# Performance work log

Hardware: AMD Instinct MI355X
Metric: run time of the kernel (lower is better)

The kernel has to match this reference:

```python
import jax, jax.numpy as jnp
import numpy as np

N_GRAPHS, GRAPH_SIZE = 64, 1024
N = N_GRAPHS * GRAPH_SIZE
IN_DIM, WIDTH, EMB, PROP, SPACE, K, NCONV = 34, 126, 128, 32, 4, 8, 5
NUM_CLASSES = 8


def _mlp4(x, W1, b1, W23, b23, W4, b4):
    h = jax.nn.elu(x @ W1 + b1)
    h = jax.nn.elu(h @ W23[0] + b23[0])
    h = jax.nn.elu(h @ W23[1] + b23[1])
    return h @ W4 + b4


def _gravnet(x, Wh, bh, Ws, bs, Wo, bo):
    # x: (N, EMB). GravNetConv: project to learned space, kNN within each graph,
    # messages h_j * exp(-10*d^2), aggregate [mean, max], concat with x, linear.
    h = x @ Wh + bh                                   # (N, PROP)
    s = x @ Ws + bs                                   # (N, SPACE)
    sg = s.reshape(N_GRAPHS, GRAPH_SIZE, SPACE)
    hg = h.reshape(N_GRAPHS, GRAPH_SIZE, PROP)
    sn2 = jnp.sum(sg * sg, -1)                        # (G,S)
    d2 = sn2[:, :, None] + sn2[:, None, :] - 2.0 * jnp.einsum('gid,gjd->gij', sg, sg)
    _, idx = jax.lax.top_k(-jax.lax.stop_gradient(d2), K)   # (G,S,K) incl. self
    s_nb = jax.vmap(lambda a, i: a[i])(sg, idx)       # (G,S,K,SPACE)
    h_nb = jax.vmap(lambda a, i: a[i])(hg, idx)       # (G,S,K,PROP)
    d2k = jnp.sum((sg[:, :, None, :] - s_nb) ** 2, -1)
    w = jnp.exp(-10.0 * d2k)                          # (G,S,K)
    msg = h_nb * w[..., None]
    agg = jnp.concatenate([msg.mean(2), msg.max(2)], -1).reshape(N, 2 * PROP)
    return jnp.concatenate([x, agg], -1) @ Wo + bo    # (N, EMB)


def _run_convs(emb, Wh, bh, Ws, bs, Wo, bo):
    # params have leading dim NCONV; convs are chained (layer i feeds layer i+1)
    def step(carry, p):
        out = _gravnet(carry, *p)
        return out, out
    _, outs = jax.lax.scan(step, emb, (Wh, bh, Ws, bs, Wo, bo))
    return outs  # (NCONV, N, EMB)


def _forward(x, n0W1, n0b1, n0W23, n0b23, n0W4, n0b4,
             cWh, cbh, cWs, cbs, cWo, cbo,
             HW1, Hb1, HW23, Hb23, Wid, bid, Wreg, breg, Wch, bch):
    emb = _mlp4(x, n0W1, n0b1, n0W23, n0b23, n0W4, n0b4)   # (N, EMB)
    # two independent conv stacks (id, reg) share the embedding input
    outs = jax.vmap(_run_convs, in_axes=(None, 0, 0, 0, 0, 0, 0))(
        emb, cWh, cbh, cWs, cbs, cWo, cbo)                  # (2, NCONV, N, EMB)
    f_id = jnp.concatenate([x, outs[0].transpose(1, 0, 2).reshape(N, NCONV * EMB)], -1)
    f_rg = jnp.concatenate([x, outs[1].transpose(1, 0, 2).reshape(N, NCONV * EMB)], -1)
    preds_id = _mlp4(f_id, HW1[0], Hb1[0], HW23[0], Hb23[0], Wid, bid)
    preds_mom = _mlp4(f_rg, HW1[1], Hb1[1], HW23[1], Hb23[1], Wreg, breg) + x[:, 1:5]
    pred_charge = _mlp4(f_rg, HW1[2], Hb1[2], HW23[2], Hb23[2], Wch, bch)
    return preds_id, preds_mom, pred_charge


def setup_inputs() -> dict:
    key = jax.random.key(0)
    ks = jax.random.split(key, 16)
    def W(i, shape):
        return jax.random.normal(ks[i], shape, jnp.float32) / np.float32(np.sqrt(shape[-2]))
    def b(shape):
        return jnp.zeros(shape, jnp.float32)
    FEAT = IN_DIM + NCONV * EMB
    return dict(
        x=jax.random.normal(ks[0], (N, IN_DIM), jnp.float32),
        batch=(jnp.arange(N) // GRAPH_SIZE).astype(jnp.int32),
        n0W1=W(1, (IN_DIM, WIDTH)), n0b1=b((WIDTH,)),
        n0W23=W(2, (2, WIDTH, WIDTH)), n0b23=b((2, WIDTH)),
        n0W4=W(3, (WIDTH, EMB)), n0b4=b((EMB,)),
        cWh=W(4, (2, NCONV, EMB, PROP)), cbh=b((2, NCONV, PROP)),
        cWs=W(5, (2, NCONV, EMB, SPACE)), cbs=b((2, NCONV, SPACE)),
        cWo=W(6, (2, NCONV, EMB + 2 * PROP, EMB)), cbo=b((2, NCONV, EMB)),
        HW1=W(7, (3, FEAT, WIDTH)), Hb1=b((3, WIDTH)),
        HW23=W(8, (3, 2, WIDTH, WIDTH)), Hb23=b((3, 2, WIDTH)),
        Wid=W(9, (WIDTH, NUM_CLASSES)), bid=b((NUM_CLASSES,)),
        Wreg=W(10, (WIDTH, 4)), breg=b((4,)),
        Wch=W(11, (WIDTH, 1)), bch=b((1,)),
    )


def reference(x, batch, n0W1, n0b1, n0W23, n0b23, n0W4, n0b4,
              cWh, cbh, cWs, cbs, cWo, cbo,
              HW1, Hb1, HW23, Hb23, Wid, bid, Wreg, breg, Wch, bch):
    # `batch` is implied by the fixed (N_GRAPHS, GRAPH_SIZE) layout used in _gravnet
    return _forward(x, n0W1, n0b1, n0W23, n0b23, n0W4, n0b4,
                    cWh, cbh, cWs, cbs, cWo, cbo,
                    HW1, Hb1, HW23, Hb23, Wid, bid, Wreg, breg, Wch, bch)
```

## Files before the change

kernel.cpp:

```cpp
#include <hip/hip_runtime.h>
#include <hip/hip_bf16.h>
#include <cstdint>

#define N_TOT 65536
#define NG 64
#define GS 1024
#define IN_DIM 34
#define WIDTH 126
#define EMB 128
#define PROP 32
#define SPACE 4
#define KNN 8
#define NCONV 5
#define FEAT (IN_DIM + NCONV*EMB)
#define FLDB 680
#define CATW (EMB + 2*PROP)
#define AGGW (2*PROP)
#define PRJW 36

typedef __attribute__((ext_vector_type(8))) short short8v;
typedef __attribute__((ext_vector_type(4))) float f32x4;

__device__ __forceinline__ unsigned short f2bf(float f){
  unsigned int u = __float_as_uint(f);
  unsigned int r = (u + 0x7FFFu + ((u >> 16) & 1u)) >> 16;
  return (unsigned short)r;
}
__device__ __forceinline__ float bf2f(unsigned short b){
  return __uint_as_float(((unsigned int)b) << 16);
}

struct WDesc {
  const float* s1; const float* s2;
  int ld1, ld2, nc1, K, Nn, limbs, ncp;
  long long dstoff;
};
#define NMAT 32
struct WDescs { WDesc d[NMAT]; };

__global__ __launch_bounds__(256)
void conv_weights_kernel(WDescs DS, unsigned short* __restrict__ pool)
{
  int m = blockIdx.y;
  WDesc d = DS.d[m];
  if (d.K == 0) return;
  int ntiles = (d.K + 31) >> 5;
  int ncp = d.ncp;
  int nchunk = ncp >> 5;
  int kt = blockIdx.x / nchunk;
  int cc = blockIdx.x % nchunk;
  if (kt >= ntiles) return;
  int t = threadIdx.x;
  int kk = t & 31;
  int k = kt*32 + kk;
  for (int c = (t >> 5); c < 32; c += 8){
    int col = cc*32 + c;
    float v = 0.f;
    if (k < d.K && col < d.Nn)
      v = (col < d.nc1) ? d.s1[(size_t)k*d.ld1 + col]
                        : d.s2[(size_t)k*d.ld2 + (col - d.nc1)];
    for (int l = 0; l < d.limbs; ++l){
      unsigned short b = f2bf(v); v -= bf2f(b);
      pool[d.dstoff + ((long long)(l*ntiles + kt)*ncp + col)*32 + kk] = b;
    }
  }
}

__global__ __launch_bounds__(256)
void xconv_kernel(const float* __restrict__ x, unsigned short* __restrict__ featb)
{
  int idx = blockIdx.x*256 + threadIdx.x;
  if (idx < N_TOT*IN_DIM){
    int r = idx / IN_DIM, c = idx - r*IN_DIM;
    featb[(size_t)r*FLDB + c] = f2bf(x[idx]);
  }
}

template<int LIMBS, int ABF, int NT>
__global__ __launch_bounds__(256)
void mfma_gemm(const void* __restrict__ A1v, int lda1, int K1,
               const float* __restrict__ A2, int lda2, int K2,
               const unsigned short* __restrict__ BL, int ncp,
               const float* __restrict__ bias1, const float* __restrict__ bias2,
               int bsplit,
               float* __restrict__ C, int ldc, int Nn, int mode, int act,
               unsigned short* __restrict__ Cb, int ldcb)
{
  constexpr int ASTR = LIMBS*32 + 8;
  constexpr int RB = (NT == 128) ? 4 : 2;
  __shared__ __align__(16) unsigned short Alds[128*ASTR];
  const float* A1 = (const float*)A1v;
  const unsigned short* Ab = (const unsigned short*)A1v;

  const int K = K1 + K2;
  const int ntiles = (K + 31) >> 5;
  const int t = threadIdx.x;
  const int bm0 = blockIdx.x * 128;
  const int col0 = blockIdx.y * NT;
  const int lane = t & 63;
  const int wid  = t >> 6;
  const int wr = (NT == 128) ? (wid >> 1) * 64 : wid * 32;
  const int wc = (NT == 128) ? (wid & 1) * 64 : 0;
  const int frow = lane & 15;
  const int fk   = (lane >> 4) * 8;
  const int a_row = t >> 1;
  const int a_kh  = (t & 1) * 16;
  const size_t rr = (size_t)(bm0 + a_row);

  float v[16];
  short8v pb0, pb1;

  auto loadreg = [&](int kt){
    const int k0 = kt * 32;
    if (ABF){
      if (k0 + 31 < K){
        pb0 = *(const short8v*)&Ab[rr*lda1 + k0 + a_kh];
        pb1 = *(const short8v*)&Ab[rr*lda1 + k0 + a_kh + 8];
      } else {
        #pragma unroll
        for (int j = 0; j < 8; ++j){
          int ka = k0 + a_kh + j;
          pb0[j] = (ka < K) ? (short)Ab[rr*lda1 + ka] : (short)0;
        }
        #pragma unroll
        for (int j = 0; j < 8; ++j){
          int ka = k0 + a_kh + 8 + j;
          pb1[j] = (ka < K) ? (short)Ab[rr*lda1 + ka] : (short)0;
        }
      }
    } else {
      #pragma unroll
      for (int j = 0; j < 16; ++j){
        int ka = k0 + a_kh + j;
        float xv = 0.f;
        if (ka < K)
          xv = (ka < K1) ? A1[rr*lda1 + ka] : A2[rr*lda2 + (ka - K1)];
        v[j] = xv;
      }
    }
  };

  auto storelds = [&](){
    if (ABF){
      *(short8v*)&Alds[a_row*ASTR + a_kh]     = pb0;
      *(short8v*)&Alds[a_row*ASTR + a_kh + 8] = pb1;
    } else {
      #pragma unroll
      for (int l = 0; l < LIMBS; ++l){
        short8v q0, q1;
        #pragma unroll
        for (int j = 0; j < 8; ++j){
          unsigned short b = f2bf(v[j]); v[j] -= bf2f(b); q0[j] = (short)b;
        }
        #pragma unroll
        for (int j = 0; j < 8; ++j){
          unsigned short b = f2bf(v[8+j]); v[8+j] -= bf2f(b); q1[j] = (short)b;
        }
        *(short8v*)&Alds[a_row*ASTR + l*32 + a_kh]     = q0;
        *(short8v*)&Alds[a_row*ASTR + l*32 + a_kh + 8] = q1;
      }
    }
  };

  f32x4 acc[RB][4];
  #pragma unroll
  for (int i = 0; i < RB; ++i)
    #pragma unroll
    for (int j = 0; j < 4; ++j)
      acc[i][j] = (f32x4){0.f, 0.f, 0.f, 0.f};

  loadreg(0);
  for (int kt = 0; kt < ntiles; ++kt){
    __syncthreads();
    storelds();
    if (kt + 1 < ntiles) loadreg(kt + 1);
    __syncthreads();
    #pragma unroll
    for (int lA = 0; lA < LIMBS; ++lA){
      short8v af[RB];
      #pragma unroll
      for (int rb = 0; rb < RB; ++rb)
        af[rb] = *(const short8v*)&Alds[(wr + rb*16 + frow)*ASTR + lA*32 + fk];
      #pragma unroll
      for (int lB = 0; lB < LIMBS - lA; ++lB){
        const unsigned short* bbase =
            BL + ((long long)(lB*ntiles + kt)*ncp)*32;
        short8v bfr[4];
        #pragma unroll
        for (int cb = 0; cb < 4; ++cb){
          int col = col0 + wc + cb*16 + frow;
          bfr[cb] = *(const short8v*)&bbase[(long long)col*32 + fk];
        }
        #pragma unroll
        for (int rb = 0; rb < RB; ++rb)
          #pragma unroll
          for (int cb = 0; cb < 4; ++cb)
            acc[rb][cb] = __builtin_amdgcn_mfma_f32_16x16x32_bf16(
                af[rb], bfr[cb], acc[rb][cb], 0, 0, 0);
      }
    }
  }

  const int lr4 = (lane >> 4) * 4;
  #pragma unroll
  for (int rb = 0; rb < RB; ++rb){
    #pragma unroll
    for (int cb = 0; cb < 4; ++cb){
      const int col = col0 + wc + cb*16 + frow;
      if (col < Nn){
        float bv = 0.f;
        if (bias1) bv = (col < bsplit) ? bias1[col] : bias2[col - bsplit];
        #pragma unroll
        for (int ri = 0; ri < 4; ++ri){
          const size_t row = (size_t)(bm0 + wr + rb*16 + lr4 + ri);
          float vv = acc[rb][cb][ri];
          if (mode == 1){
            C[row*ldc + col] += vv;
          } else if (mode == 2){
            float a2 = vv + C[row*ldc + col] + bv;
            C[row*ldc + col] = (a2 > 0.f) ? a2 : expm1f(a2);
          } else {
            if (bias1) vv += bv;
            if (act == 1) vv = (vv > 0.f) ? vv : expm1f(vv);
            C[row*ldc + col] = vv;
            if (Cb) Cb[row*(size_t)ldcb + col] = f2bf(vv);
          }
        }
      }
    }
  }
}

template<int BM, int BN, int BK, int TM, int TN>
__global__ __launch_bounds__(256)
void gemm_tile_kernel(const float* __restrict__ A1, int lda1, int K1,
                      const float* __restrict__ W, const float* __restrict__ bias,
                      float* __restrict__ C, int ldc, int Nn, int act,
                      const float* __restrict__ addx, int addx_ld, int addx_off)
{
  constexpr int LDA = BM + 4;
  constexpr int LDB = BN + 4;
  constexpr int APASS = (BM*BK)/1024;
  constexpr int BPASS = (BN*BK)/1024;
  constexpr int AROWS = 256/(BK/4);
  constexpr int BROWS = 256/(BN/4);
  __shared__ float As[BK*LDA];
  __shared__ float Bs[BK*LDB];
  const int K = K1;
  const int t = threadIdx.x;
  const int bm0 = blockIdx.x * BM;
  const int bn0 = blockIdx.y * BN;
  const int tx = t % 16;
  const int ty = t / 16;
  const int a_r = t / (BK/4);
  const int a_k = 4 * (t % (BK/4));
  const int b_c = t % (BN/4);
  const int b_k = t / (BN/4);

  float ar[APASS][4], br[BPASS][4];
  auto load_tile = [&](int k0){
    #pragma unroll
    for (int p = 0; p < APASS; ++p){
      size_t rr = (size_t)(bm0 + a_r + p*AROWS);
      #pragma unroll
      for (int j = 0; j < 4; ++j){
        int ka = k0 + a_k + j;
        ar[p][j] = (ka < K) ? A1[rr*lda1 + ka] : 0.f;
      }
    }
    #pragma unroll
    for (int p = 0; p < BPASS; ++p){
      int kb = k0 + b_k + p*BROWS;
      #pragma unroll
      for (int j = 0; j < 4; ++j){
        int col = bn0 + 4*b_c + j;
        br[p][j] = (kb < K && col < Nn) ? W[(size_t)kb*Nn + col] : 0.f;
      }
    }
  };
  auto store_tile = [&](){
    #pragma unroll
    for (int p = 0; p < APASS; ++p)
      #pragma unroll
      for (int j = 0; j < 4; ++j)
        As[(a_k + j)*LDA + a_r + p*AROWS] = ar[p][j];
    #pragma unroll
    for (int p = 0; p < BPASS; ++p)
      *(float4*)&Bs[(b_k + p*BROWS)*LDB + 4*b_c] =
          make_float4(br[p][0], br[p][1], br[p][2], br[p][3]);
  };

  float acc[TM][TN];
  #pragma unroll
  for (int i = 0; i < TM; ++i)
    #pragma unroll
    for (int j = 0; j < TN; ++j) acc[i][j] = 0.f;

  auto compute_tile = [&](){
    #pragma unroll
    for (int kk = 0; kk < BK; ++kk){
      float a[TM], b[TN];
      #pragma unroll
      for (int iq = 0; iq < TM/4; ++iq){
        float4 v = *(const float4*)&As[kk*LDA + iq*(BM/2) + 4*ty];
        a[iq*4+0] = v.x; a[iq*4+1] = v.y; a[iq*4+2] = v.z; a[iq*4+3] = v.w;
      }
      #pragma unroll
      for (int jq = 0; jq < TN/4; ++jq){
        float4 v = *(const float4*)&Bs[kk*LDB + jq*(BN/2) + 4*tx];
        b[jq*4+0] = v.x; b[jq*4+1] = v.y; b[jq*4+2] = v.z; b[jq*4+3] = v.w;
      }
      #pragma unroll
      for (int i = 0; i < TM; ++i)
        #pragma unroll
        for (int j = 0; j < TN; ++j)
          acc[i][j] += a[i]*b[j];
    }
  };

  const int ntiles = (K + BK - 1)/BK;
  load_tile(0); store_tile(); __syncthreads();
  for (int tt = 1; tt < ntiles; ++tt){
    load_tile(tt*BK);
    compute_tile();
    __syncthreads();
    store_tile();
    __syncthreads();
  }
  compute_tile();

  #pragma unroll
  for (int i = 0; i < TM; ++i){
    size_t row = (size_t)(bm0 + (i/4)*(BM/2) + 4*ty + (i%4));
    #pragma unroll
    for (int j = 0; j < TN; ++j){
      int col = bn0 + (j/4)*(BN/2) + 4*tx + (j%4);
      if (col < Nn){
        float v = acc[i][j];
        if (bias) v += bias[col];
        if (act == 1) v = (v > 0.f) ? v : expm1f(v);
        if (addx) v += addx[row*addx_ld + addx_off + col];
        C[row*ldc + col] = v;
      }
    }
  }
}

__global__ __launch_bounds__(256)
void knn_agg_kernel(const float* __restrict__ proj, float* __restrict__ agg)
{
  __shared__ float4 ssv[GS];
  __shared__ float  sn2[GS];
  __shared__ float  cd[4][64][KNN];
  __shared__ int    ci[4][64][KNN];
  __shared__ float  wl[64][KNN];

  const int g   = blockIdx.x >> 4;
  const int seg = blockIdx.x & 15;
  const int t = threadIdx.x;
  const int wave = t >> 6;
  const int lane = t & 63;

  const float* pg = proj + (size_t)g*GS*PRJW;
  for (int i = t; i < GS; i += 256){
    float4 v = *(const float4*)(pg + (size_t)i*PRJW + PROP);
    ssv[i] = v;
    sn2[i] = v.x*v.x + v.y*v.y + v.z*v.z + v.w*v.w;
  }
  __syncthreads();

  const int i = seg*64 + lane;
  float4 sv = ssv[i];
  float myn2 = sn2[i];
  float si0 = sv.x, si1 = sv.y, si2 = sv.z, si3 = sv.w;

  float bd[KNN]; int bi[KNN];
  #pragma unroll
  for (int k = 0; k < KNN; ++k){ bd[k] = 1e30f; bi[k] = 0; }

  const int jbeg = wave * 256;
  for (int j0 = jbeg; j0 < jbeg + 256; j0 += 8){
    float dv[8];
    #pragma unroll
    for (int u = 0; u < 8; ++u){
      float4 sj = ssv[j0+u];
      float dot = si0*sj.x + si1*sj.y + si2*sj.z + si3*sj.w;
      dv[u] = myn2 + sn2[j0+u] - 2.f*dot;
    }
    float mn = fminf(fminf(fminf(dv[0],dv[1]), fminf(dv[2],dv[3])),
                     fminf(fminf(dv[4],dv[5]), fminf(dv[6],dv[7])));
    if (mn < bd[KNN-1]){
      #pragma unroll
      for (int u = 0; u < 8; ++u){
        float d2 = dv[u];
        if (d2 < bd[KNN-1]){
          int j = j0 + u;
          #pragma unroll
          for (int q = KNN-1; q >= 1; --q){
            bool cq = d2 < bd[q];
            bool cp = d2 < bd[q-1];
            float nv = cp ? bd[q-1] : d2;
            int   ni = cp ? bi[q-1] : j;
            if (cq){ bd[q] = nv; bi[q] = ni; }
          }
          if (d2 < bd[0]){ bd[0] = d2; bi[0] = j; }
        }
      }
    }
  }
  #pragma unroll
  for (int k = 0; k < KNN; ++k){ cd[wave][lane][k] = bd[k]; ci[wave][lane][k] = bi[k]; }
  __syncthreads();

  if (wave == 0){
    #pragma unroll
    for (int c = 1; c < 4; ++c){
      #pragma unroll
      for (int k = 0; k < KNN; ++k){
        float d2 = cd[c][lane][k];
        if (d2 < bd[KNN-1]){
          int j = ci[c][lane][k];
          #pragma unroll
          for (int q = KNN-1; q >= 1; --q){
            bool cq = d2 < bd[q];
            bool cp = d2 < bd[q-1];
            float nv = cp ? bd[q-1] : d2;
            int   ni = cp ? bi[q-1] : j;
            if (cq){ bd[q] = nv; bi[q] = ni; }
          }
          if (d2 < bd[0]){ bd[0] = d2; bi[0] = j; }
        }
      }
    }
    #pragma unroll
    for (int k = 0; k < KNN; ++k){ cd[0][lane][k] = bd[k]; ci[0][lane][k] = bi[k]; }
  }
  __syncthreads();

  {
    const int r = t & 63;
    float4 si_ = ssv[seg*64 + r];
    #pragma unroll
    for (int kx = (t >> 6); kx < KNN; kx += 4){
      int j = ci[0][r][kx];
      float4 sj = ssv[j];
      float d0 = si_.x - sj.x, d1 = si_.y - sj.y;
      float d2_ = si_.z - sj.z, d3 = si_.w - sj.w;
      float dd = d0*d0 + d1*d1 + d2_*d2_ + d3*d3;
      wl[r][kx] = expf(-10.f*dd);
    }
  }
  __syncthreads();

  {
    const int r = t & 63;
    const int q = t >> 6;
    float msum[8], mmax[8];
    #pragma unroll
    for (int u = 0; u < 8; ++u){ msum[u] = 0.f; mmax[u] = -1e30f; }
    #pragma unroll
    for (int k = 0; k < KNN; ++k){
      int j = ci[0][r][k];
      float wk = wl[r][k];
      const float* hr = pg + (size_t)j*PRJW + q*8;
      float4 h0 = *(const float4*)(hr);
      float4 h1 = *(const float4*)(hr + 4);
      float v0 = h0.x*wk, v1 = h0.y*wk, v2 = h0.z*wk, v3 = h0.w*wk;
      float v4 = h1.x*wk, v5 = h1.y*wk, v6 = h1.z*wk, v7 = h1.w*wk;
      msum[0]+=v0; mmax[0]=fmaxf(mmax[0],v0);
      msum[1]+=v1; mmax[1]=fmaxf(mmax[1],v1);
      msum[2]+=v2; mmax[2]=fmaxf(mmax[2],v2);
      msum[3]+=v3; mmax[3]=fmaxf(mmax[3],v3);
      msum[4]+=v4; mmax[4]=fmaxf(mmax[4],v4);
      msum[5]+=v5; mmax[5]=fmaxf(mmax[5],v5);
      msum[6]+=v6; mmax[6]=fmaxf(mmax[6],v6);
      msum[7]+=v7; mmax[7]=fmaxf(mmax[7],v7);
    }
    float* arow = agg + ((size_t)g*GS + seg*64 + r)*AGGW;
    #pragma unroll
    for (int u = 0; u < 8; ++u){
      arow[q*8 + u]        = msum[u]*(1.f/KNN);
      arow[PROP + q*8 + u] = mmax[u];
    }
  }
}

extern "C" void kernel_launch(void* const* d_in, const int* in_sizes, int n_in,
                              void* d_out, int out_size, void* d_ws, size_t ws_size,
                              hipStream_t stream)
{
  const float* x     = (const float*)d_in[0];
  const float* n0W1  = (const float*)d_in[2];
  const float* n0b1  = (const float*)d_in[3];
  const float* n0W23 = (const float*)d_in[4];
  const float* n0b23 = (const float*)d_in[5];
  const float* n0W4  = (const float*)d_in[6];
  const float* n0b4  = (const float*)d_in[7];
  const float* cWh   = (const float*)d_in[8];
  const float* cbh   = (const float*)d_in[9];
  const float* cWs   = (const float*)d_in[10];
  const float* cbs   = (const float*)d_in[11];
  const float* cWo   = (const float*)d_in[12];
  const float* cbo   = (const float*)d_in[13];
  const float* HW1   = (const float*)d_in[14];
  const float* Hb1   = (const float*)d_in[15];
  const float* HW23  = (const float*)d_in[16];
  const float* Hb23  = (const float*)d_in[17];
  const float* Wid   = (const float*)d_in[18];
  const float* bid   = (const float*)d_in[19];
  const float* Wreg  = (const float*)d_in[20];
  const float* breg  = (const float*)d_in[21];
  const float* Wch   = (const float*)d_in[22];
  const float* bch   = (const float*)d_in[23];
  float* out = (float*)d_out;
  (void)in_sizes; (void)n_in; (void)out_size;

  char* wsp = (char*)d_ws;
  unsigned short* featb = (unsigned short*)(wsp);
  float* P     = (float*)(wsp + 89128960);
  float* Q     = (float*)(wsp + 122683392);
  float* projb = (float*)(wsp + 156237824);
  float* aggb  = (float*)(wsp + 165675008);
  unsigned short* pool = (unsigned short*)(wsp + 182452224);
  float* hacc  = P;
  float* t1    = (float*)wsp;

  WDescs DS{};
  long long woff = 0; int nd = 0;
  auto addm = [&](const float* s1, const float* s2, int ld1, int ld2,
                  int nc1, int K, int Nn, int limbs, int nalign)->long long {
    int ntiles = (K + 31) >> 5;
    int ncp = (Nn + nalign - 1) & ~(nalign - 1);
    long long o = woff;
    DS.d[nd].s1 = s1; DS.d[nd].s2 = s2; DS.d[nd].ld1 = ld1; DS.d[nd].ld2 = ld2;
    DS.d[nd].nc1 = nc1; DS.d[nd].K = K; DS.d[nd].Nn = Nn; DS.d[nd].limbs = limbs;
    DS.d[nd].ncp = ncp; DS.d[nd].dstoff = o; nd++;
    woff += (long long)limbs * ntiles * ncp * 32;
    return o;
  };
  long long o_e1 = addm(n0W1, nullptr, WIDTH, 0, WIDTH, IN_DIM, WIDTH, 3, 128);
  long long o_e2 = addm(n0W23, nullptr, WIDTH, 0, WIDTH, WIDTH, WIDTH, 3, 128);
  long long o_e3 = addm(n0W23 + WIDTH*WIDTH, nullptr, WIDTH, 0, WIDTH, WIDTH, WIDTH, 3, 128);
  long long o_e4 = addm(n0W4, nullptr, EMB, 0, EMB, WIDTH, EMB, 3, 128);
  long long o_pj[10], o_wo[10];
  for (int p = 0; p < 10; ++p){
    o_pj[p] = addm(cWh + (size_t)p*EMB*PROP, cWs + (size_t)p*EMB*SPACE,
                   PROP, SPACE, PROP, EMB, PRJW, 3, 64);
    o_wo[p] = addm(cWo + (size_t)p*CATW*EMB, nullptr, EMB, 0, EMB, CATW, EMB, 3, 128);
  }
  long long o_L1s0  = addm(HW1, nullptr, WIDTH, 0, WIDTH, FEAT, WIDTH, 1, 128);
  long long o_L1s12 = addm(HW1 + (size_t)1*FEAT*WIDTH, HW1 + (size_t)2*FEAT*WIDTH,
                           WIDTH, WIDTH, WIDTH, FEAT, 2*WIDTH, 1, 128);
  long long o_hh[6];
  for (int q = 0; q < 6; ++q)
    o_hh[q] = addm(HW23 + (size_t)q*WIDTH*WIDTH, nullptr, WIDTH, 0, WIDTH, WIDTH, WIDTH, 1, 128);

  long long E_off = ((182452224LL + woff*2) + 255) & ~255LL;
  bool haveE = (E_off + (long long)N_TOT*EMB*4 <= (long long)ws_size);
  float* E = (float*)(wsp + E_off);

  hipLaunchKernelGGL(conv_weights_kernel, dim3(176, NMAT), dim3(256), 0, stream, DS, pool);

  auto gemmM = [&](int limbs, int abf, int nt, const void* A1, int lda1, int K1,
                   const float* A2, int lda2, int K2,
                   long long boff, int ncp,
                   const float* b1, const float* b2, int bsplit,
                   float* C, int ldc, int Nn, int mode, int act,
                   unsigned short* Cb, int ldcb){
    dim3 grid(N_TOT/128, ncp/nt);
    if (limbs == 3 && nt == 64)
      hipLaunchKernelGGL((mfma_gemm<3,0,64>), grid, dim3(256), 0, stream,
          A1, lda1, K1, A2, lda2, K2, pool + boff, ncp, b1, b2, bsplit,
          C, ldc, Nn, mode, act, Cb, ldcb);
    else if (limbs == 3)
      hipLaunchKernelGGL((mfma_gemm<3,0,128>), grid, dim3(256), 0, stream,
          A1, lda1, K1, A2, lda2, K2, pool + boff, ncp, b1, b2, bsplit,
          C, ldc, Nn, mode, act, Cb, ldcb);
    else if (abf)
      hipLaunchKernelGGL((mfma_gemm<1,1,128>), grid, dim3(256), 0, stream,
          A1, lda1, K1, A2, lda2, K2, pool + boff, ncp, b1, b2, bsplit,
          C, ldc, Nn, mode, act, Cb, ldcb);
    else
      hipLaunchKernelGGL((mfma_gemm<1,0,128>), grid, dim3(256), 0, stream,
          A1, lda1, K1, A2, lda2, K2, pool + boff, ncp, b1, b2, bsplit,
          C, ldc, Nn, mode, act, Cb, ldcb);
  };
  auto gemmS = [&](const float* A1, int lda1, int K1,
                   const float* W, const float* b,
                   float* C, int ldc, int Nn, int act,
                   const float* addx, int addx_ld, int addx_off){
    dim3 grid(N_TOT/64, (Nn+63)/64);
    hipLaunchKernelGGL((gemm_tile_kernel<64,64,32,4,4>), grid, dim3(256), 0, stream,
        A1, lda1, K1, W, b, C, ldc, Nn, act, addx, addx_ld, addx_off);
  };
  const int BIG = 1 << 30;

  auto run_embedding = [&](float* dst){
    gemmM(3,0,128, x, IN_DIM, IN_DIM, nullptr,0,0, o_e1, 128, n0b1, nullptr, BIG,
          Q, EMB, WIDTH, 0, 1, nullptr, 0);
    gemmM(3,0,128, Q, EMB, WIDTH, nullptr,0,0, o_e2, 128, n0b23, nullptr, BIG,
          P, EMB, WIDTH, 0, 1, nullptr, 0);
    gemmM(3,0,128, P, EMB, WIDTH, nullptr,0,0, o_e3, 128, n0b23 + WIDTH, nullptr, BIG,
          Q, EMB, WIDTH, 0, 1, nullptr, 0);
    gemmM(3,0,128, Q, EMB, WIDTH, nullptr,0,0, o_e4, 128, n0b4, nullptr, BIG,
          dst, EMB, EMB, 0, 0, nullptr, 0);
  };

  if (haveE) run_embedding(E);

  for (int s = 0; s < 2; ++s){
    hipLaunchKernelGGL(xconv_kernel, dim3((N_TOT*IN_DIM + 255)/256), dim3(256),
                       0, stream, x, featb);
    if (!haveE) run_embedding(P);

    float* cur = haveE ? E : P;
    float* b0  = haveE ? P : Q;
    float* b1  = haveE ? Q : P;

    for (int cv = 0; cv < NCONV; ++cv){
      int pidx = s*NCONV + cv;
      float* nxt = (cv & 1) ? b1 : b0;
      gemmM(3,0,64, cur, EMB, EMB, nullptr,0,0, o_pj[pidx], 64,
            cbh + pidx*PROP, cbs + pidx*SPACE, PROP,
            projb, PRJW, PRJW, 0, 0, nullptr, 0);
      hipLaunchKernelGGL(knn_agg_kernel, dim3(NG*16), dim3(256), 0, stream,
                         projb, aggb);
      gemmM(3,0,128, cur, EMB, EMB, aggb, AGGW, AGGW, o_wo[pidx], 128,
            cbo + pidx*EMB, nullptr, BIG, nxt, EMB, EMB, 0, 0,
            featb + IN_DIM + cv*EMB, FLDB);
      cur = nxt;
    }

    if (s == 0){
      gemmM(1,1,128, featb, FLDB, FEAT, nullptr,0,0, o_L1s0, 128,
            Hb1, nullptr, BIG, hacc, WIDTH, WIDTH, 0, 1, nullptr, 0);
    } else {
      gemmM(1,1,128, featb, FLDB, FEAT, nullptr,0,0, o_L1s12, 256,
            Hb1 + WIDTH, Hb1 + 2*WIDTH, WIDTH,
            hacc, 2*WIDTH, 2*WIDTH, 0, 1, nullptr, 0);
    }

    auto finish_head = [&](int hidx, float* ha, int lda_ha,
                           float* dst, int dst_ld, int out_dim,
                           const float* Wl, const float* bl,
                           const float* addx, int addx_ld, int addx_off){
      gemmM(1,0,128, ha, lda_ha, WIDTH, nullptr,0,0, o_hh[hidx*2+0], 128,
            Hb23 + (hidx*2+0)*WIDTH, nullptr, BIG,
            t1, WIDTH, WIDTH, 0, 1, nullptr, 0);
      gemmM(1,0,128, t1, WIDTH, WIDTH, nullptr,0,0, o_hh[hidx*2+1], 128,
            Hb23 + (hidx*2+1)*WIDTH, nullptr, BIG,
            ha, lda_ha, WIDTH, 0, 1, nullptr, 0);
      gemmS(ha, lda_ha, WIDTH, Wl, bl, dst, dst_ld, out_dim, 0,
            addx, addx_ld, addx_off);
    };

    if (s == 0){
      finish_head(0, hacc, WIDTH, out, 8, 8, Wid, bid, nullptr, 0, 0);
    } else {
      finish_head(1, hacc, 2*WIDTH, out + (size_t)N_TOT*8, 4, 4,
                  Wreg, breg, x, IN_DIM, 1);
      finish_head(2, hacc + WIDTH, 2*WIDTH, out + (size_t)N_TOT*12, 1, 1,
                  Wch, bch, nullptr, 0, 0);
    }
  }
}
```

Baseline: 2.355 ms.

## Fuse Wo GEMM with next-layer projection and shrink MFMA GEMM row tile

Adds a fused kernel that computes the GravNet output linear layer and then, from the result kept in LDS as three bf16 limbs, the next conv's h/s projection. This removes one separate projection GEMM launch per conv and the re-read of the new embedding from global memory. The generic MFMA GEMM row tile drops from 128 to 64 rows per block and the unused accumulate modes are removed, giving more blocks and less LDS per block at the cost of more B-fragment reloads. The knn kernel's block-to-graph mapping is also reordered so consecutive blocks cover different graphs.

```diff
diff --git a/kernel.cpp b/kernel.cpp
--- a/kernel.cpp
+++ b/kernel.cpp
@@ -18,15 +18,16 @@
 #define AGGW (2*PROP)
 #define PRJW 36
 
+typedef unsigned short ushort;
 typedef __attribute__((ext_vector_type(8))) short short8v;
 typedef __attribute__((ext_vector_type(4))) float f32x4;
 
-__device__ __forceinline__ unsigned short f2bf(float f){
+__device__ __forceinline__ ushort f2bf(float f){
   unsigned int u = __float_as_uint(f);
   unsigned int r = (u + 0x7FFFu + ((u >> 16) & 1u)) >> 16;
-  return (unsigned short)r;
+  return (ushort)r;
 }
-__device__ __forceinline__ float bf2f(unsigned short b){
+__device__ __forceinline__ float bf2f(ushort b){
   return __uint_as_float(((unsigned int)b) << 16);
 }
 
@@ -39,7 +40,7 @@
 struct WDescs { WDesc d[NMAT]; };
 
 __global__ __launch_bounds__(256)
-void conv_weights_kernel(WDescs DS, unsigned short* __restrict__ pool)
+void conv_weights_kernel(WDescs DS, ushort* __restrict__ pool)
 {
   int m = blockIdx.y;
   WDesc d = DS.d[m];
@@ -60,14 +61,14 @@
       v = (col < d.nc1) ? d.s1[(size_t)k*d.ld1 + col]
                         : d.s2[(size_t)k*d.ld2 + (col - d.nc1)];
     for (int l = 0; l < d.limbs; ++l){
-      unsigned short b = f2bf(v); v -= bf2f(b);
+      ushort b = f2bf(v); v -= bf2f(b);
       pool[d.dstoff + ((long long)(l*ntiles + kt)*ncp + col)*32 + kk] = b;
     }
   }
 }
 
 __global__ __launch_bounds__(256)
-void xconv_kernel(const float* __restrict__ x, unsigned short* __restrict__ featb)
+void xconv_kernel(const float* __restrict__ x, ushort* __restrict__ featb)
 {
   int idx = blockIdx.x*256 + threadIdx.x;
   if (idx < N_TOT*IN_DIM){
@@ -80,57 +81,51 @@
 __global__ __launch_bounds__(256)
 void mfma_gemm(const void* __restrict__ A1v, int lda1, int K1,
                const float* __restrict__ A2, int lda2, int K2,
-               const unsigned short* __restrict__ BL, int ncp,
+               const ushort* __restrict__ BL, int ncp,
                const float* __restrict__ bias1, const float* __restrict__ bias2,
                int bsplit,
-               float* __restrict__ C, int ldc, int Nn, int mode, int act,
-               unsigned short* __restrict__ Cb, int ldcb)
+               float* __restrict__ C, int ldc, int Nn, int act,
+               ushort* __restrict__ Cb, int ldcb)
 {
   constexpr int ASTR = LIMBS*32 + 8;
-  constexpr int RB = (NT == 128) ? 4 : 2;
-  __shared__ __align__(16) unsigned short Alds[128*ASTR];
+  constexpr int CB = (NT == 128) ? 4 : 2;
+  __shared__ __align__(16) ushort Alds[64*ASTR];
   const float* A1 = (const float*)A1v;
-  const unsigned short* Ab = (const unsigned short*)A1v;
+  const ushort* Ab = (const ushort*)A1v;
 
   const int K = K1 + K2;
   const int ntiles = (K + 31) >> 5;
   const int t = threadIdx.x;
-  const int bm0 = blockIdx.x * 128;
+  const int bm0 = blockIdx.x * 64;
   const int col0 = blockIdx.y * NT;
   const int lane = t & 63;
   const int wid  = t >> 6;
-  const int wr = (NT == 128) ? (wid >> 1) * 64 : wid * 32;
-  const int wc = (NT == 128) ? (wid & 1) * 64 : 0;
+  const int wr = (wid >> 1) * 32;
+  const int wc = (wid & 1) * (NT/2);
   const int frow = lane & 15;
   const int fk   = (lane >> 4) * 8;
-  const int a_row = t >> 1;
-  const int a_kh  = (t & 1) * 16;
+  const int a_row = t >> 2;
+  const int a_kh  = (t & 3) * 8;
   const size_t rr = (size_t)(bm0 + a_row);
 
-  float v[16];
-  short8v pb0, pb1;
+  float v[8];
+  short8v pb0;
 
   auto loadreg = [&](int kt){
     const int k0 = kt * 32;
     if (ABF){
-      if (k0 + 31 < K){
+      if (k0 + a_kh + 7 < K){
         pb0 = *(const short8v*)&Ab[rr*lda1 + k0 + a_kh];
-        pb1 = *(const short8v*)&Ab[rr*lda1 + k0 + a_kh + 8];
       } else {
         #pragma unroll
         for (int j = 0; j < 8; ++j){
           int ka = k0 + a_kh + j;
           pb0[j] = (ka < K) ? (short)Ab[rr*lda1 + ka] : (short)0;
         }
-        #pragma unroll
-        for (int j = 0; j < 8; ++j){
-          int ka = k0 + a_kh + 8 + j;
-          pb1[j] = (ka < K) ? (short)Ab[rr*lda1 + ka] : (short)0;
-        }
       }
     } else {
       #pragma unroll
-      for (int j = 0; j < 16; ++j){
+      for (int j = 0; j < 8; ++j){
         int ka = k0 + a_kh + j;
         float xv = 0.f;
         if (ka < K)
@@ -139,34 +134,27 @@
       }
     }
   };
-
   auto storelds = [&](){
     if (ABF){
-      *(short8v*)&Alds[a_row*ASTR + a_kh]     = pb0;
-      *(short8v*)&Alds[a_row*ASTR + a_kh + 8] = pb1;
+      *(short8v*)&Alds[a_row*ASTR + a_kh] = pb0;
     } else {
       #pragma unroll
       for (int l = 0; l < LIMBS; ++l){
-        short8v q0, q1;
+        short8v q0;
         #pragma unroll
         for (int j = 0; j < 8; ++j){
-          unsigned short b = f2bf(v[j]); v[j] -= bf2f(b); q0[j] = (short)b;
+          ushort b = f2bf(v[j]); v[j] -= bf2f(b); q0[j] = (short)b;
         }
-        #pragma unroll
-        for (int j = 0; j < 8; ++j){
-          unsigned short b = f2bf(v[8+j]); v[8+j] -= bf2f(b); q1[j] = (short)b;
-        }
-        *(short8v*)&Alds[a_row*ASTR + l*32 + a_kh]     = q0;
-        *(short8v*)&Alds[a_row*ASTR + l*32 + a_kh + 8] = q1;
-      }
-    }
-  };
-
-  f32x4 acc[RB][4];
-  #pragma unroll
-  for (int i = 0; i < RB; ++i)
-    #pragma unroll
-    for (int j = 0; j < 4; ++j)
+        *(short8v*)&Alds[a_row*ASTR + l*32 + a_kh] = q0;
+      }
+    }
+  };
+
+  f32x4 acc[2][CB];
+  #pragma unroll
+  for (int i = 0; i < 2; ++i)
+    #pragma unroll
+    for (int j = 0; j < CB; ++j)
       acc[i][j] = (f32x4){0.f, 0.f, 0.f, 0.f};
 
   loadreg(0);
@@ -177,24 +165,23 @@
     __syncthreads();
     #pragma unroll
     for (int lA = 0; lA < LIMBS; ++lA){
-      short8v af[RB];
-      #pragma unroll
-      for (int rb = 0; rb < RB; ++rb)
+      short8v af[2];
+      #pragma unroll
+      for (int rb = 0; rb < 2; ++rb)
         af[rb] = *(const short8v*)&Alds[(wr + rb*16 + frow)*ASTR + lA*32 + fk];
       #pragma unroll
       for (int lB = 0; lB < LIMBS - lA; ++lB){
-        const unsigned short* bbase =
-            BL + ((long long)(lB*ntiles + kt)*ncp)*32;
-        short8v bfr[4];
+        const ushort* bbase = BL + ((long long)(lB*ntiles + kt)*ncp)*32;
+        short8v bfr[CB];
         #pragma unroll
-        for (int cb = 0; cb < 4; ++cb){
+        for (int cb = 0; cb < CB; ++cb){
           int col = col0 + wc + cb*16 + frow;
           bfr[cb] = *(const short8v*)&bbase[(long long)col*32 + fk];
         }
         #pragma unroll
-        for (int rb = 0; rb < RB; ++rb)
+        for (int rb = 0; rb < 2; ++rb)
           #pragma unroll
-          for (int cb = 0; cb < 4; ++cb)
+          for (int cb = 0; cb < CB; ++cb)
             acc[rb][cb] = __builtin_amdgcn_mfma_f32_16x16x32_bf16(
                 af[rb], bfr[cb], acc[rb][cb], 0, 0, 0);
       }
@@ -203,9 +190,9 @@
 
   const int lr4 = (lane >> 4) * 4;
   #pragma unroll
-  for (int rb = 0; rb < RB; ++rb){
-    #pragma unroll
-    for (int cb = 0; cb < 4; ++cb){
+  for (int rb = 0; rb < 2; ++rb){
+    #pragma unroll
+    for (int cb = 0; cb < CB; ++cb){
       const int col = col0 + wc + cb*16 + frow;
       if (col < Nn){
         float bv = 0.f;
@@ -214,18 +201,157 @@
         for (int ri = 0; ri < 4; ++ri){
           const size_t row = (size_t)(bm0 + wr + rb*16 + lr4 + ri);
           float vv = acc[rb][cb][ri];
-          if (mode == 1){
-            C[row*ldc + col] += vv;
-          } else if (mode == 2){
-            float a2 = vv + C[row*ldc + col] + bv;
-            C[row*ldc + col] = (a2 > 0.f) ? a2 : expm1f(a2);
-          } else {
-            if (bias1) vv += bv;
-            if (act == 1) vv = (vv > 0.f) ? vv : expm1f(vv);
-            C[row*ldc + col] = vv;
-            if (Cb) Cb[row*(size_t)ldcb + col] = f2bf(vv);
-          }
+          if (bias1) vv += bv;
+          if (act == 1) vv = (vv > 0.f) ? vv : expm1f(vv);
+          C[row*ldc + col] = vv;
+          if (Cb) Cb[row*(size_t)ldcb + col] = f2bf(vv);
         }
+      }
+    }
+  }
+}
+
+__global__ __launch_bounds__(256)
+void fused_wo_proj(const float* __restrict__ cur,
+                   const float* __restrict__ agg,
+                   const ushort* __restrict__ BLwo,
+                   const float* __restrict__ cbo_,
+                   const ushort* __restrict__ BLpj,
+                   const float* __restrict__ cbh_, const float* __restrict__ cbs_,
+                   float* __restrict__ nxt,
+                   ushort* __restrict__ fslot, int ldcb,
+                   float* __restrict__ projb_)
+{
+  constexpr int ASTR = 104;
+  __shared__ __align__(16) ushort Alds[64*ASTR];
+  __shared__ __align__(16) ushort PL[64*4*104];
+
+  const int t = threadIdx.x;
+  const int bm0 = blockIdx.x * 64;
+  const int lane = t & 63;
+  const int wid  = t >> 6;
+  const int wr = (wid >> 1) * 32;
+  const int wc = (wid & 1) * 64;
+  const int frow = lane & 15;
+  const int fk   = (lane >> 4) * 8;
+  const int lr4  = (lane >> 4) * 4;
+  const int a_row = t >> 2;
+  const int a_kh  = (t & 3) * 8;
+  const size_t rr = (size_t)(bm0 + a_row);
+
+  float v[8];
+  auto loadreg = [&](int kt){
+    const int k0 = kt * 32;
+    #pragma unroll
+    for (int j = 0; j < 8; ++j){
+      int ka = k0 + a_kh + j;
+      v[j] = (ka < EMB) ? cur[rr*EMB + ka] : agg[rr*AGGW + (ka - EMB)];
+    }
+  };
+  auto storelds = [&](){
+    #pragma unroll
+    for (int l = 0; l < 3; ++l){
+      short8v q0;
+      #pragma unroll
+      for (int j = 0; j < 8; ++j){
+        ushort b = f2bf(v[j]); v[j] -= bf2f(b); q0[j] = (short)b;
+      }
+      *(short8v*)&Alds[a_row*ASTR + l*32 + a_kh] = q0;
+    }
+  };
+
+  f32x4 acc[2][4];
+  #pragma unroll
+  for (int i = 0; i < 2; ++i)
+    #pragma unroll
+    for (int j = 0; j < 4; ++j)
+      acc[i][j] = (f32x4){0.f, 0.f, 0.f, 0.f};
+
+  loadreg(0);
+  for (int kt = 0; kt < 6; ++kt){
+    __syncthreads();
+    storelds();
+    if (kt + 1 < 6) loadreg(kt + 1);
+    __syncthreads();
+    #pragma unroll
+    for (int lA = 0; lA < 3; ++lA){
+      short8v af[2];
+      #pragma unroll
+      for (int rb = 0; rb < 2; ++rb)
+        af[rb] = *(const short8v*)&Alds[(wr + rb*16 + frow)*ASTR + lA*32 + fk];
+      #pragma unroll
+      for (int lB = 0; lB < 3 - lA; ++lB){
+        const ushort* bbase = BLwo + ((long long)(lB*6 + kt)*128)*32;
+        short8v bfr[4];
+        #pragma unroll
+        for (int cb = 0; cb < 4; ++cb){
+          int col = wc + cb*16 + frow;
+          bfr[cb] = *(const short8v*)&bbase[(long long)col*32 + fk];
+        }
+        #pragma unroll
+        for (int rb = 0; rb < 2; ++rb)
+          #pragma unroll
+          for (int cb = 0; cb < 4; ++cb)
+            acc[rb][cb] = __builtin_amdgcn_mfma_f32_16x16x32_bf16(
+                af[rb], bfr[cb], acc[rb][cb], 0, 0, 0);
+      }
+    }
+  }
+  __syncthreads();
+
+  #pragma unroll
+  for (int rb = 0; rb < 2; ++rb){
+    #pragma unroll
+    for (int cb = 0; cb < 4; ++cb){
+      const int col = wc + cb*16 + frow;
+      const float bv = cbo_[col];
+      #pragma unroll
+      for (int ri = 0; ri < 4; ++ri){
+        const int lr = wr + rb*16 + lr4 + ri;
+        const size_t row = (size_t)(bm0 + lr);
+        float vv = acc[rb][cb][ri] + bv;
+        nxt[row*EMB + col] = vv;
+        fslot[row*(size_t)ldcb + col] = f2bf(vv);
+        ushort l0 = f2bf(vv); float r0 = vv - bf2f(l0);
+        ushort l1 = f2bf(r0); r0 -= bf2f(l1);
+        ushort l2 = f2bf(r0);
+        const int kt2 = col >> 5, kk = col & 31;
+        PL[lr*416 + kt2*104 + kk]      = l0;
+        PL[lr*416 + kt2*104 + 32 + kk] = l1;
+        PL[lr*416 + kt2*104 + 64 + kk] = l2;
+      }
+    }
+  }
+  __syncthreads();
+
+  const int r0 = wid * 16;
+  f32x4 p[4];
+  #pragma unroll
+  for (int j = 0; j < 4; ++j) p[j] = (f32x4){0.f, 0.f, 0.f, 0.f};
+  for (int kt2 = 0; kt2 < 4; ++kt2){
+    #pragma unroll
+    for (int lA = 0; lA < 3; ++lA){
+      short8v af = *(const short8v*)&PL[(r0 + frow)*416 + kt2*104 + lA*32 + fk];
+      #pragma unroll
+      for (int lB = 0; lB < 3 - lA; ++lB){
+        const ushort* bb = BLpj + ((long long)(lB*4 + kt2)*64)*32;
+        #pragma unroll
+        for (int cb = 0; cb < 4; ++cb){
+          short8v bf_ = *(const short8v*)&bb[(long long)(cb*16 + frow)*32 + fk];
+          p[cb] = __builtin_amdgcn_mfma_f32_16x16x32_bf16(af, bf_, p[cb], 0, 0, 0);
+        }
+      }
+    }
+  }
+  #pragma unroll
+  for (int cb = 0; cb < 4; ++cb){
+    const int col = cb*16 + frow;
+    if (col < PRJW){
+      const float bv = (col < PROP) ? cbh_[col] : cbs_[col - PROP];
+      #pragma unroll
+      for (int ri = 0; ri < 4; ++ri){
+        const size_t row = (size_t)(bm0 + r0 + lr4 + ri);
+        projb_[row*PRJW + col] = p[cb][ri] + bv;
       }
     }
   }
@@ -355,8 +481,8 @@
   __shared__ int    ci[4][64][KNN];
   __shared__ float  wl[64][KNN];
 
-  const int g   = blockIdx.x >> 4;
-  const int seg = blockIdx.x & 15;
+  const int g   = blockIdx.x & 63;
+  const int seg = blockIdx.x >> 6;
   const int t = threadIdx.x;
   const int wave = t >> 6;
   const int lane = t & 63;
@@ -516,12 +642,12 @@
   (void)in_sizes; (void)n_in; (void)out_size;
 
   char* wsp = (char*)d_ws;
-  unsigned short* featb = (unsigned short*)(wsp);
+  ushort* featb = (ushort*)(wsp);
   float* P     = (float*)(wsp + 89128960);
   float* Q     = (float*)(wsp + 122683392);
   float* projb = (float*)(wsp + 156237824);
   float* aggb  = (float*)(wsp + 165675008);
-  unsigned short* pool = (unsigned short*)(wsp + 182452224);
+  ushort* pool = (ushort*)(wsp + 182452224);
   float* hacc  = P;
   float* t1    = (float*)wsp;
 
@@ -565,25 +691,25 @@
                    const float* A2, int lda2, int K2,
                    long long boff, int ncp,
                    const float* b1, const float* b2, int bsplit,
-                   float* C, int ldc, int Nn, int mode, int act,
-                   unsigned short* Cb, int ldcb){
-    dim3 grid(N_TOT/128, ncp/nt);
+                   float* C, int ldc, int Nn, int act,
+                   ushort* Cb, int ldcb){
+    dim3 grid(N_TOT/64, ncp/nt);
     if (limbs == 3 && nt == 64)
       hipLaunchKernelGGL((mfma_gemm<3,0,64>), grid, dim3(256), 0, stream,
           A1, lda1, K1, A2, lda2, K2, pool + boff, ncp, b1, b2, bsplit,
-          C, ldc, Nn, mode, act, Cb, ldcb);
+          C, ldc, Nn, act, Cb, ldcb);
     else if (limbs == 3)
       hipLaunchKernelGGL((mfma_gemm<3,0,128>), grid, dim3(256), 0, stream,
           A1, lda1, K1, A2, lda2, K2, pool + boff, ncp, b1, b2, bsplit,
-          C, ldc, Nn, mode, act, Cb, ldcb);
+          C, ldc, Nn, act, Cb, ldcb);
     else if (abf)
       hipLaunchKernelGGL((mfma_gemm<1,1,128>), grid, dim3(256), 0, stream,
           A1, lda1, K1, A2, lda2, K2, pool + boff, ncp, b1, b2, bsplit,
-          C, ldc, Nn, mode, act, Cb, ldcb);
+          C, ldc, Nn, act, Cb, ldcb);
     else
       hipLaunchKernelGGL((mfma_gemm<1,0,128>), grid, dim3(256), 0, stream,
           A1, lda1, K1, A2, lda2, K2, pool + boff, ncp, b1, b2, bsplit,
-          C, ldc, Nn, mode, act, Cb, ldcb);
+          C, ldc, Nn, act, Cb, ldcb);
   };
   auto gemmS = [&](const float* A1, int lda1, int K1,
                    const float* W, const float* b,
@@ -597,13 +723,13 @@
 
   auto run_embedding = [&](float* dst){
     gemmM(3,0,128, x, IN_DIM, IN_DIM, nullptr,0,0, o_e1, 128, n0b1, nullptr, BIG,
-          Q, EMB, WIDTH, 0, 1, nullptr, 0);
+          Q, EMB, WIDTH, 1, nullptr, 0);
     gemmM(3,0,128, Q, EMB, WIDTH, nullptr,0,0, o_e2, 128, n0b23, nullptr, BIG,
-          P, EMB, WIDTH, 0, 1, nullptr, 0);
+          P, EMB, WIDTH, 1, nullptr, 0);
     gemmM(3,0,128, P, EMB, WIDTH, nullptr,0,0, o_e3, 128, n0b23 + WIDTH, nullptr, BIG,
-          Q, EMB, WIDTH, 0, 1, nullptr, 0);
+          Q, EMB, WIDTH, 1, nullptr, 0);
     gemmM(3,0,128, Q, EMB, WIDTH, nullptr,0,0, o_e4, 128, n0b4, nullptr, BIG,
-          dst, EMB, EMB, 0, 0, nullptr, 0);
+          dst, EMB, EMB, 0, nullptr, 0);
   };
 
   if (haveE) run_embedding(E);
@@ -617,27 +743,36 @@
     float* b0  = haveE ? P : Q;
     float* b1  = haveE ? Q : P;
 
+    gemmM(3,0,64, cur, EMB, EMB, nullptr,0,0, o_pj[s*NCONV], 64,
+          cbh + (s*NCONV)*PROP, cbs + (s*NCONV)*SPACE, PROP,
+          projb, PRJW, PRJW, 0, nullptr, 0);
+
     for (int cv = 0; cv < NCONV; ++cv){
       int pidx = s*NCONV + cv;
       float* nxt = (cv & 1) ? b1 : b0;
-      gemmM(3,0,64, cur, EMB, EMB, nullptr,0,0, o_pj[pidx], 64,
-            cbh + pidx*PROP, cbs + pidx*SPACE, PROP,
-            projb, PRJW, PRJW, 0, 0, nullptr, 0);
       hipLaunchKernelGGL(knn_agg_kernel, dim3(NG*16), dim3(256), 0, stream,
                          projb, aggb);
-      gemmM(3,0,128, cur, EMB, EMB, aggb, AGGW, AGGW, o_wo[pidx], 128,
-            cbo + pidx*EMB, nullptr, BIG, nxt, EMB, EMB, 0, 0,
-            featb + IN_DIM + cv*EMB, FLDB);
+      if (cv < NCONV-1){
+        int pnx = pidx + 1;
+        hipLaunchKernelGGL(fused_wo_proj, dim3(N_TOT/64), dim3(256), 0, stream,
+            cur, aggb, pool + o_wo[pidx], cbo + pidx*EMB,
+            pool + o_pj[pnx], cbh + pnx*PROP, cbs + pnx*SPACE,
+            nxt, featb + IN_DIM + cv*EMB, FLDB, projb);
+      } else {
+        gemmM(3,0,128, cur, EMB, EMB, aggb, AGGW, AGGW, o_wo[pidx], 128,
+              cbo + pidx*EMB, nullptr, BIG, nxt, EMB, EMB, 0,
+              featb + IN_DIM + cv*EMB, FLDB);
+      }
       cur = nxt;
     }
 
     if (s == 0){
       gemmM(1,1,128, featb, FLDB, FEAT, nullptr,0,0, o_L1s0, 128,
-            Hb1, nullptr, BIG, hacc, WIDTH, WIDTH, 0, 1, nullptr, 0);
+            Hb1, nullptr, BIG, hacc, WIDTH, WIDTH, 1, nullptr, 0);
     } else {
       gemmM(1,1,128, featb, FLDB, FEAT, nullptr,0,0, o_L1s12, 256,
             Hb1 + WIDTH, Hb1 + 2*WIDTH, WIDTH,
-            hacc, 2*WIDTH, 2*WIDTH, 0, 1, nullptr, 0);
+            hacc, 2*WIDTH, 2*WIDTH, 1, nullptr, 0);
     }
 
     auto finish_head = [&](int hidx, float* ha, int lda_ha,
@@ -646,10 +781,10 @@
                            const float* addx, int addx_ld, int addx_off){
       gemmM(1,0,128, ha, lda_ha, WIDTH, nullptr,0,0, o_hh[hidx*2+0], 128,
             Hb23 + (hidx*2+0)*WIDTH, nullptr, BIG,
-            t1, WIDTH, WIDTH, 0, 1, nullptr, 0);
+            t1, WIDTH, WIDTH, 1, nullptr, 0);
       gemmM(1,0,128, t1, WIDTH, WIDTH, nullptr,0,0, o_hh[hidx*2+1], 128,
             Hb23 + (hidx*2+1)*WIDTH, nullptr, BIG,
-            ha, lda_ha, WIDTH, 0, 1, nullptr, 0);
+            ha, lda_ha, WIDTH, 1, nullptr, 0);
       gemmS(ha, lda_ha, WIDTH, Wl, bl, dst, dst_ld, out_dim, 0,
             addx, addx_ld, addx_off);
     };
```

Result: faster. 1.886 ms, median of 2 (-19.9%).
